# Optimization experiments

Hardware: AMD Instinct MI355X
Metric: run time of the kernel (lower is better)

The kernel has to match this reference:

```python
import jax, jax.numpy as jnp
import numpy as np

N = 50000        # nodes
E = 1600000      # edges (avg degree 32)
D = 64           # emb_dim
H = 2            # heads
NEG_SLOPE = 0.2
BOND_VOCAB = 5   # vocab per bond feature (3 categorical features)


def setup_inputs() -> dict:
    key = jax.random.key(0)
    ks = jax.random.split(key, 8)
    x = jax.random.normal(ks[0], (N, D), jnp.float32)
    edge_index = jax.random.randint(ks[1], (2, E), 0, N)
    edge_attr = jax.random.randint(ks[2], (E, 3), 0, BOND_VOCAB)
    W = jax.random.normal(ks[3], (D, H * D), jnp.float32) / np.float32(np.sqrt(D))
    b_W = jnp.zeros((H * D,), jnp.float32)
    att = jax.random.normal(ks[4], (1, H, 2 * D), jnp.float32) * 0.1
    bias = jnp.zeros((D,), jnp.float32)
    bond_emb = jax.random.normal(ks[5], (3, BOND_VOCAB, H * D), jnp.float32) * 0.1
    return dict(x=x, edge_index=edge_index, edge_attr=edge_attr,
                W=W, b_W=b_W, att=att, bias=bias, bond_emb=bond_emb)


def reference(x, edge_index, edge_attr, W, b_W, att, bias, bond_emb):
    row, col = edge_index[0], edge_index[1]  # src (x_j), dst (x_i / aggregation target)
    # BondEncoder: sum of per-feature categorical embeddings -> [E, H*D]
    e = (bond_emb[0][edge_attr[:, 0]]
         + bond_emb[1][edge_attr[:, 1]]
         + bond_emb[2][edge_attr[:, 2]])
    h = x @ W + b_W                                   # [N, H*D]
    x_j = h[row].reshape(-1, H, D) + e.reshape(-1, H, D)   # message source + edge emb
    x_i = h[col].reshape(-1, H, D)                         # message target
    # attention logits: [E, H]
    alpha = (jnp.concatenate([x_i, x_j], axis=-1) * att).sum(-1)
    alpha = jnp.where(alpha >= 0, alpha, NEG_SLOPE * alpha)  # leaky_relu
    # segment softmax over edge_index[0] (source node), PyG semantics
    m = jax.ops.segment_max(alpha, row, num_segments=N)      # [N, H]
    m = jnp.where(jnp.isfinite(m), m, 0.0)                   # empty segments -> 0
    ea = jnp.exp(alpha - m[row])
    s = jax.ops.segment_sum(ea, row, num_segments=N)
    alpha = ea / (s[row] + 1e-16)
    # weighted messages, scatter-add to destination nodes
    msg = x_j * alpha[:, :, None]                            # [E, H, D]
    aggr = jax.ops.segment_sum(msg, col, num_segments=N)     # [N, H, D]
    # update: mean over heads + bias
    return aggr.mean(axis=1) + bias
```

## Files before the change

### kernel.cpp

```cpp
#include <hip/hip_runtime.h>
#include <hip/hip_bf16.h>
#include <math.h>

#define NEG_SLOPE 0.2f
#define CHUNK 2048
#define NPB2 128
#define SCAP 5120

__device__ __forceinline__ unsigned f2bf(float f) {
  unsigned u = __float_as_uint(f);
  return (u + 0x7fffu + ((u >> 16) & 1u)) >> 16;
}

__global__ __launch_bounds__(256) void k1_gemm(
    const float* __restrict__ x, const float* __restrict__ W,
    const float* __restrict__ bW, const float* __restrict__ att,
    unsigned int* __restrict__ hb, float* __restrict__ ai,
    float* __restrict__ aj, int Nn) {
  int t = threadIdx.x;
  int lane = t & 63;
  int wid = blockIdx.x * (blockDim.x >> 6) + (t >> 6);
  int nwaves = gridDim.x * (blockDim.x >> 6);

  float Wr0[64], Wr1[64];
#pragma unroll
  for (int k = 0; k < 64; ++k) {
    Wr0[k] = W[k * 128 + lane];
    Wr1[k] = W[k * 128 + 64 + lane];
  }
  float bs0 = bW[lane], bs1 = bW[64 + lane];
  float ati0 = att[lane];
  float atj0 = att[64 + lane];
  float ati1 = att[128 + lane];
  float atj1 = att[192 + lane];

  for (int row = wid; row < Nn; row += nwaves) {
    int r = __builtin_amdgcn_readfirstlane(row);
    const float* __restrict__ xr = x + (size_t)r * 64;
    float a0a = 0.f, a0b = 0.f, a1a = 0.f, a1b = 0.f;
#pragma unroll
    for (int k = 0; k < 64; k += 2) {
      float xk0 = xr[k], xk1 = xr[k + 1];
      a0a = fmaf(xk0, Wr0[k], a0a);
      a1a = fmaf(xk0, Wr1[k], a1a);
      a0b = fmaf(xk1, Wr0[k + 1], a0b);
      a1b = fmaf(xk1, Wr1[k + 1], a1b);
    }
    float h0 = a0a + a0b + bs0;
    float h1 = a1a + a1b + bs1;
    hb[(size_t)r * 64 + lane] = f2bf(h0) | (f2bf(h1) << 16);

    float ti0 = ati0 * h0, tj0 = atj0 * h0;
    float ti1 = ati1 * h1, tj1 = atj1 * h1;
    ti0 += __shfl_xor(ti0, 32, 64);
    tj0 += __shfl_xor(tj0, 32, 64);
    ti1 += __shfl_xor(ti1, 32, 64);
    tj1 += __shfl_xor(tj1, 32, 64);
    float mi = (lane < 32) ? ti0 : ti1;
    float mj = (lane < 32) ? tj0 : tj1;
#pragma unroll
    for (int off = 16; off > 0; off >>= 1) {
      mi += __shfl_xor(mi, off, 64);
      mj += __shfl_xor(mj, off, 64);
    }
    if ((lane & 31) == 0) {
      ai[r * 2 + (lane >> 5)] = mi;
      aj[r * 2 + (lane >> 5)] = mj;
    }
  }
}

__global__ __launch_bounds__(256) void k_bin(
    const int* __restrict__ ei, const int* __restrict__ eattr,
    unsigned int* __restrict__ rec, int* __restrict__ cnt_tbl,
    int* __restrict__ base_tbl, unsigned int* __restrict__ rec_src,
    int* __restrict__ cnt_tbl2, int* __restrict__ base_tbl2, int Ee, int NCB) {
  __shared__ unsigned sbuf[CHUNK];
  __shared__ unsigned sbuf2[CHUNK];
  __shared__ int hist[512], cur[512], hist2[512], cur2[512];
  int t = threadIdx.x;
  for (int i = t; i < NCB; i += 256) { hist[i] = 0; hist2[i] = 0; }
  __syncthreads();
  int start = blockIdx.x * CHUNK;
  int end = min(start + CHUNK, Ee);
  int cnt = end - start;
  int cbv[CHUNK / 256], cb2v[CHUNK / 256];
  unsigned pkv[CHUNK / 256], pk2v[CHUNK / 256];
  int nk = 0;
  for (int e = start + t; e < end; e += 256, ++nk) {
    int dst = __builtin_nontemporal_load(&ei[Ee + e]);
    int src = __builtin_nontemporal_load(&ei[e]);
    int a0 = __builtin_nontemporal_load(&eattr[e * 3]);
    int a1 = __builtin_nontemporal_load(&eattr[e * 3 + 1]);
    int a2 = __builtin_nontemporal_load(&eattr[e * 3 + 2]);
    unsigned c012 = (unsigned)(a0 + 5 * a1 + 25 * a2);
    cbv[nk] = dst >> 7;
    pkv[nk] = (unsigned)src | (c012 << 16) | ((unsigned)(dst & 127) << 23);
    cb2v[nk] = src >> 7;
    pk2v[nk] = (unsigned)dst | ((unsigned)(src & 127) << 17) | (c012 << 24);
    atomicAdd(&hist[dst >> 7], 1);
    atomicAdd(&hist2[src >> 7], 1);
  }
  __syncthreads();
  if (t == 0) {
    int s = 0;
    for (int i = 0; i < NCB; ++i) { cur[i] = s; s += hist[i]; }
  }
  if (t == 64) {
    int s = 0;
    for (int i = 0; i < NCB; ++i) { cur2[i] = s; s += hist2[i]; }
  }
  __syncthreads();
  for (int i = t; i < NCB; i += 256) {
    cnt_tbl[blockIdx.x * NCB + i] = hist[i];
    base_tbl[blockIdx.x * NCB + i] = cur[i];
    cnt_tbl2[blockIdx.x * NCB + i] = hist2[i];
    base_tbl2[blockIdx.x * NCB + i] = cur2[i];
  }
  __syncthreads();
  for (int k = 0; k < nk; ++k) {
    int pos = atomicAdd(&cur[cbv[k]], 1);
    sbuf[pos] = pkv[k];
    int pos2 = atomicAdd(&cur2[cb2v[k]], 1);
    sbuf2[pos2] = pk2v[k];
  }
  __syncthreads();
  for (int i = t; i < cnt; i += 256) {
    __builtin_nontemporal_store(sbuf[i], &rec[start + i]);
    __builtin_nontemporal_store(sbuf2[i], &rec_src[start + i]);
  }
}

__global__ __launch_bounds__(256) void k_segoff_a(
    const int* __restrict__ cnt_tbl, int* __restrict__ segdst,
    int* __restrict__ btot, int NCB, int NBLK) {
  __shared__ int s[256];
  int t = threadIdx.x, cb = blockIdx.x;
  int per = (NBLK + 255) / 256;
  int loc[8];
  int sum = 0;
  for (int j = 0; j < per; ++j) {
    int blk = t * per + j;
    int v = (blk < NBLK) ? cnt_tbl[blk * NCB + cb] : 0;
    loc[j] = sum;
    sum += v;
  }
  s[t] = sum;
  __syncthreads();
#pragma unroll
  for (int o = 1; o < 256; o <<= 1) {
    int xv = (t >= o) ? s[t - o] : 0;
    __syncthreads();
    s[t] += xv;
    __syncthreads();
  }
  int excl = s[t] - sum;
  for (int j = 0; j < per; ++j) {
    int blk = t * per + j;
    if (blk < NBLK) segdst[cb * NBLK + blk] = excl + loc[j];
  }
  if (t == 255) btot[cb] = s[255];
}

__global__ __launch_bounds__(512) void k_segoff_b(
    const int* __restrict__ btot, int* __restrict__ coarse_base, int NCB, int Ee) {
  __shared__ int s[512];
  int t = threadIdx.x;
  int v = (t < NCB) ? btot[t] : 0;
  s[t] = v;
  __syncthreads();
#pragma unroll
  for (int o = 1; o < 512; o <<= 1) {
    int xv = (t >= o) ? s[t - o] : 0;
    __syncthreads();
    s[t] += xv;
    __syncthreads();
  }
  if (t < NCB) coarse_base[t] = s[t] - v;
  if (t == 0) coarse_base[NCB] = Ee;
}

__global__ __launch_bounds__(256) void k_sacc(
    const unsigned int* __restrict__ rec_src, const int* __restrict__ cnt_tbl2,
    const int* __restrict__ base_tbl2, const int* __restrict__ segdst2,
    const int* __restrict__ btot2, const float2* __restrict__ ai2,
    const float2* __restrict__ aj2, const float* __restrict__ att,
    const float* __restrict__ bemb, float* __restrict__ sden,
    int Nn, int NCB, int NBLK) {
  __shared__ unsigned ubuf[SCAP];
  __shared__ float sdl[NPB2 * 2];
  __shared__ float2 ajs[NPB2];
  __shared__ float tbl[30];
  int t = threadIdx.x;
  int cb = blockIdx.x;
  if (t < 30) {
    int f = t / 10, rem = t % 10, c = rem >> 1, hh = rem & 1;
    float sacc = 0.f;
    for (int d = 0; d < 64; ++d)
      sacc += att[hh * 128 + 64 + d] * bemb[(f * 5 + c) * 128 + hh * 64 + d];
    tbl[t] = sacc;
  }
  int node0 = cb << 7;
  if (t < NPB2 && node0 + t < Nn) ajs[t] = aj2[node0 + t];
  sdl[t] = 0.f;
  int total = btot2[cb];
  __syncthreads();
  bool fits = (total <= SCAP);

#define SACC_BODY(U, AIV)                                                      \
  {                                                                            \
    int sl = ((U) >> 17) & 127;                                                \
    int c012 = ((U) >> 24) & 127;                                              \
    int a0 = c012 % 5, a1 = (c012 / 5) % 5, a2 = c012 / 25;                    \
    float2 ajv = ajs[sl];                                                      \
    float lg0 = AIV.x + ajv.x + tbl[a0 * 2] + tbl[10 + a1 * 2] +               \
                tbl[20 + a2 * 2];                                              \
    float lg1 = AIV.y + ajv.y + tbl[a0 * 2 + 1] + tbl[10 + a1 * 2 + 1] +       \
                tbl[20 + a2 * 2 + 1];                                          \
    lg0 = lg0 >= 0.f ? lg0 : NEG_SLOPE * lg0;                                  \
    lg1 = lg1 >= 0.f ? lg1 : NEG_SLOPE * lg1;                                  \
    atomicAdd(&sdl[sl * 2], __expf(lg0));                                      \
    atomicAdd(&sdl[sl * 2 + 1], __expf(lg1));                                  \
  }

  if (fits) {
    for (int blk = t; blk < NBLK; blk += 256) {
      int len = cnt_tbl2[blk * NCB + cb];
      if (!len) continue;
      int sp = blk * CHUNK + base_tbl2[blk * NCB + cb];
      int dp = segdst2[cb * NBLK + blk];
      for (int j = 0; j < len; ++j) ubuf[dp + j] = rec_src[sp + j];
    }
    __syncthreads();
    int i = t;
    for (; i + 3 * 256 < total; i += 4 * 256) {
      unsigned u[4];
      float2 aiv[4];
#pragma unroll
      for (int k = 0; k < 4; ++k) u[k] = ubuf[i + k * 256];
#pragma unroll
      for (int k = 0; k < 4; ++k) aiv[k] = ai2[u[k] & 0x1FFFF];
#pragma unroll
      for (int k = 0; k < 4; ++k) SACC_BODY(u[k], aiv[k])
    }
    for (; i < total; i += 256) {
      unsigned u = ubuf[i];
      float2 aiv = ai2[u & 0x1FFFF];
      SACC_BODY(u, aiv)
    }
  } else {
    for (int blk = t; blk < NBLK; blk += 256) {
      int len = cnt_tbl2[blk * NCB + cb];
      int sp = blk * CHUNK + base_tbl2[blk * NCB + cb];
      for (int j = 0; j < len; ++j) {
        unsigned u = rec_src[sp + j];
        float2 aiv = ai2[u & 0x1FFFF];
        SACC_BODY(u, aiv)
      }
    }
  }
#undef SACC_BODY
  __syncthreads();
  if (node0 + (t >> 1) < Nn) sden[(size_t)node0 * 2 + t] = sdl[t];
}

__global__ __launch_bounds__(256) void k_sort(
    const unsigned int* __restrict__ rec, const int* __restrict__ cnt_tbl,
    const int* __restrict__ base_tbl, const int* __restrict__ segdst,
    const int* __restrict__ coarse_base, const float2* __restrict__ ai2,
    const float2* __restrict__ aj2, const float2* __restrict__ sd2,
    const float* __restrict__ att, const float* __restrict__ bemb,
    unsigned int* __restrict__ eix2, float2* __restrict__ alpha2,
    int* __restrict__ off, int Nn, int NCB, int NBLK, int Ee) {
  __shared__ unsigned ubuf[SCAP];
  __shared__ unsigned ubuf2[SCAP];
  __shared__ int hist[NPB2], basex[NPB2], curx[NPB2];
  __shared__ float tbl[30];
  __shared__ float2 ais[NPB2];
  int t = threadIdx.x;
  int cb = blockIdx.x;
  if (t < 30) {
    int f = t / 10, rem = t % 10, c = rem >> 1, hh = rem & 1;
    float sacc = 0.f;
    for (int d = 0; d < 64; ++d)
      sacc += att[hh * 128 + 64 + d] * bemb[(f * 5 + c) * 128 + hh * 64 + d];
    tbl[t] = sacc;
  }
  int node0 = cb << 7;
  if (t < NPB2) {
    hist[t] = 0;
    if (node0 + t < Nn) ais[t] = ai2[node0 + t];
  }
  int gbase = coarse_base[cb];
  int total = coarse_base[cb + 1] - gbase;
  __syncthreads();
  bool fits = (total <= SCAP);

  if (fits) {
    for (int blk = t; blk < NBLK; blk += 256) {
      int len = cnt_tbl[blk * NCB + cb];
      if (!len) continue;
      int sp = blk * CHUNK + base_tbl[blk * NCB + cb];
      int dp = segdst[cb * NBLK + blk];
      for (int j = 0; j < len; ++j) ubuf[dp + j] = rec[sp + j];
    }
    __syncthreads();
    for (int i = t; i < total; i += 256)
      atomicAdd(&hist[(ubuf[i] >> 23) & 127], 1);
    __syncthreads();
    if (t == 0) {
      int s = 0;
      for (int i = 0; i < NPB2; ++i) { basex[i] = s; s += hist[i]; }
    }
    __syncthreads();
    if (t < NPB2) {
      curx[t] = basex[t];
      if (node0 + t < Nn) off[node0 + t] = gbase + basex[t];
    }
    if (cb == 0 && t == 0) off[Nn] = Ee;
    __syncthreads();
    for (int i = t; i < total; i += 256) {
      unsigned u = ubuf[i];
      int pos = atomicAdd(&curx[(u >> 23) & 127], 1);
      ubuf2[pos] = u;
    }
    __syncthreads();

#define OUT_BODY(I, U, AJV, SDV)                                               \
    {                                                                          \
      int src = (U) & 0xFFFF;                                                  \
      int c012 = ((U) >> 16) & 127;                                            \
      int dl = ((U) >> 23) & 127;                                              \
      int a0 = c012 % 5, a1 = (c012 / 5) % 5, a2 = c012 / 25;                  \
      float2 aiv = ais[dl];                                                    \
      float lg0 = aiv.x + AJV.x + tbl[a0 * 2] + tbl[10 + a1 * 2] +             \
                  tbl[20 + a2 * 2];                                            \
      float lg1 = aiv.y + AJV.y + tbl[a0 * 2 + 1] + tbl[10 + a1 * 2 + 1] +     \
                  tbl[20 + a2 * 2 + 1];                                        \
      lg0 = lg0 >= 0.f ? lg0 : NEG_SLOPE * lg0;                                \
      lg1 = lg1 >= 0.f ? lg1 : NEG_SLOPE * lg1;                                \
      eix2[gbase + (I)] = (unsigned)src | ((unsigned)a0 << 16) |               \
                          ((unsigned)a1 << 19) | ((unsigned)a2 << 22);         \
      alpha2[gbase + (I)] = make_float2(__expf(lg0) / (SDV.x + 1e-16f),        \
                                        __expf(lg1) / (SDV.y + 1e-16f));       \
    }

    int i = t;
    for (; i + 3 * 256 < total; i += 4 * 256) {
      unsigned u[4];
      float2 ajv[4], sdv[4];
#pragma unroll
      for (int k = 0; k < 4; ++k) u[k] = ubuf2[i + k * 256];
#pragma unroll
      for (int k = 0; k < 4; ++k) ajv[k] = aj2[u[k] & 0xFFFF];
#pragma unroll
      for (int k = 0; k < 4; ++k) sdv[k] = sd2[u[k] & 0xFFFF];
#pragma unroll
      for (int k = 0; k < 4; ++k) OUT_BODY(i + k * 256, u[k], ajv[k], sdv[k])
    }
    for (; i < total; i += 256) {
      unsigned u = ubuf2[i];
      float2 ajv = aj2[u & 0xFFFF];
      float2 sdv = sd2[u & 0xFFFF];
      OUT_BODY(i, u, ajv, sdv)
    }
#undef OUT_BODY
  } else {
    for (int blk = t; blk < NBLK; blk += 256) {
      int len = cnt_tbl[blk * NCB + cb];
      int sp = blk * CHUNK + base_tbl[blk * NCB + cb];
      for (int j = 0; j < len; ++j)
        atomicAdd(&hist[(rec[sp + j] >> 23) & 127], 1);
    }
    __syncthreads();
    if (t == 0) {
      int s = 0;
      for (int i = 0; i < NPB2; ++i) { basex[i] = s; s += hist[i]; }
    }
    __syncthreads();
    if (t < NPB2) {
      curx[t] = basex[t];
      if (node0 + t < Nn) off[node0 + t] = gbase + basex[t];
    }
    if (cb == 0 && t == 0) off[Nn] = Ee;
    __syncthreads();
    for (int blk = t; blk < NBLK; blk += 256) {
      int len = cnt_tbl[blk * NCB + cb];
      int sp = blk * CHUNK + base_tbl[blk * NCB + cb];
      for (int j = 0; j < len; ++j) {
        unsigned u = rec[sp + j];
        int src = u & 0xFFFF;
        int c012 = (u >> 16) & 127;
        int dl = (u >> 23) & 127;
        int a0 = c012 % 5, a1 = (c012 / 5) % 5, a2 = c012 / 25;
        float2 aiv = ais[dl];
        float2 ajv = aj2[src];
        float2 sdv = sd2[src];
        float lg0 = aiv.x + ajv.x + tbl[a0 * 2] + tbl[10 + a1 * 2] + tbl[20 + a2 * 2];
        float lg1 = aiv.y + ajv.y + tbl[a0 * 2 + 1] + tbl[10 + a1 * 2 + 1] +
                    tbl[20 + a2 * 2 + 1];
        lg0 = lg0 >= 0.f ? lg0 : NEG_SLOPE * lg0;
        lg1 = lg1 >= 0.f ? lg1 : NEG_SLOPE * lg1;
        int pos = gbase + atomicAdd(&curx[dl], 1);
        eix2[pos] = (unsigned)src | ((unsigned)a0 << 16) | ((unsigned)a1 << 19) |
                    ((unsigned)a2 << 22);
        alpha2[pos] = make_float2(__expf(lg0) / (sdv.x + 1e-16f),
                                  __expf(lg1) / (sdv.y + 1e-16f));
      }
    }
  }
}

__global__ __launch_bounds__(256) void k_gather(
    const unsigned int* __restrict__ eix, const float2* __restrict__ alpha2,
    const int* __restrict__ off, const unsigned int* __restrict__ hb,
    const float* __restrict__ bemb, const float* __restrict__ bias,
    float* __restrict__ out, int Nn) {
  __shared__ float bembs[15 * 128];
  __shared__ float wsm[4][32];
  int t = threadIdx.x;
  for (int i = t; i < 15 * 128; i += 256) bembs[i] = bemb[i];
  __syncthreads();
  int wave = t >> 6, lane = t & 63;
  int n = blockIdx.x * 4 + wave;
  if (n >= Nn) return;
  int p0 = __builtin_amdgcn_readfirstlane(off[n]);
  int p1 = __builtin_amdgcn_readfirstlane(off[n + 1]);
  int myf = lane / 5;
  int myc = lane % 5;
  bool active = lane < 15;
  float w0 = 0.f, w1 = 0.f;
  float acc0 = 0.f, acc1 = 0.f;

#define EDGE_BODY(U, HV, AL)                                                   \
  {                                                                            \
    acc0 = fmaf(AL.x, __uint_as_float((HV) << 16), acc0);                      \
    acc1 = fmaf(AL.y, __uint_as_float((HV) & 0xffff0000u), acc1);              \
    int a0 = ((U) >> 16) & 7, a1 = ((U) >> 19) & 7, a2 = ((U) >> 22) & 7;      \
    int sel = myf == 0 ? a0 : (myf == 1 ? a1 : a2);                            \
    float m = (active && myc == sel) ? 1.0f : 0.0f;                            \
    w0 = fmaf(m, AL.x, w0);                                                    \
    w1 = fmaf(m, AL.y, w1);                                                    \
  }

  int p = p0;
  for (; p + 8 <= p1; p += 8) {
    unsigned u[8], hv[8];
    float2 al[8];
#pragma unroll
    for (int k = 0; k < 8; ++k) u[k] = eix[p + k];
#pragma unroll
    for (int k = 0; k < 8; ++k) al[k] = alpha2[p + k];
#pragma unroll
    for (int k = 0; k < 8; ++k) {
      const unsigned* __restrict__ hrow = hb + ((size_t)(u[k] & 0xFFFFu) << 6);
      hv[k] = hrow[lane];
    }
#pragma unroll
    for (int k = 0; k < 8; ++k) EDGE_BODY(u[k], hv[k], al[k])
  }
  for (; p < p1; ++p) {
    unsigned u0 = eix[p];
    float2 al0 = alpha2[p];
    const unsigned* __restrict__ hrow = hb + ((size_t)(u0 & 0xFFFFu) << 6);
    unsigned hv0 = hrow[lane];
    EDGE_BODY(u0, hv0, al0)
  }
#undef EDGE_BODY

  if (active) {
    wsm[wave][lane * 2] = w0;
    wsm[wave][lane * 2 + 1] = w1;
  }
#pragma unroll
  for (int k = 0; k < 15; ++k) {
    acc0 += wsm[wave][k * 2] * bembs[k * 128 + lane];
    acc1 += wsm[wave][k * 2 + 1] * bembs[k * 128 + 64 + lane];
  }
  out[(size_t)n * 64 + lane] = 0.5f * (acc0 + acc1) + bias[lane];
}

extern "C" void kernel_launch(void* const* d_in, const int* in_sizes, int n_in,
                              void* d_out, int out_size, void* d_ws, size_t ws_size,
                              hipStream_t stream) {
  const float* x    = (const float*)d_in[0];
  const int*   ei   = (const int*)d_in[1];
  const int*   eatt = (const int*)d_in[2];
  const float* W    = (const float*)d_in[3];
  const float* bW   = (const float*)d_in[4];
  const float* att  = (const float*)d_in[5];
  const float* bias = (const float*)d_in[6];
  const float* bemb = (const float*)d_in[7];
  int Nn = in_sizes[0] / 64;
  int Ee = in_sizes[1] / 2;
  int NCB = (Nn + NPB2 - 1) / NPB2;
  int NBLK = (Ee + CHUNK - 1) / CHUNK;

  char* ws = (char*)d_ws;
  ws = (char*)(((uintptr_t)ws + 15) & ~(uintptr_t)15);
  float* aj = (float*)ws;                 ws += (size_t)Nn * 2 * 4;
  float* sden = (float*)ws;               ws += (size_t)Nn * 2 * 4;
  float* ai = (float*)ws;                 ws += (size_t)Nn * 2 * 4;
  unsigned int* hb = (unsigned int*)ws;   ws += (size_t)Nn * 64 * 4;
  unsigned int* rec = (unsigned int*)ws;  ws += (size_t)NBLK * CHUNK * 4;
  unsigned int* rec_src = (unsigned int*)ws; ws += (size_t)NBLK * CHUNK * 4;
  unsigned int* eix2 = (unsigned int*)ws; ws += (size_t)Ee * 4;
  float2* alpha2 = (float2*)ws;           ws += (size_t)Ee * 8;
  int* off = (int*)ws;                    ws += (size_t)(Nn + 1) * 4;
  int* cnt_tbl = (int*)ws;                ws += (size_t)NBLK * NCB * 4;
  int* base_tbl = (int*)ws;               ws += (size_t)NBLK * NCB * 4;
  int* cnt_tbl2 = (int*)ws;               ws += (size_t)NBLK * NCB * 4;
  int* base_tbl2 = (int*)ws;              ws += (size_t)NBLK * NCB * 4;
  int* segdst = (int*)ws;                 ws += (size_t)NCB * NBLK * 4;
  int* segdst2 = (int*)ws;                ws += (size_t)NCB * NBLK * 4;
  int* coarse_base = (int*)ws;            ws += (size_t)(NCB + 1) * 4;
  int* btot = (int*)ws;                   ws += (size_t)NCB * 4;
  int* btot2 = (int*)ws;                  ws += (size_t)NCB * 4;

  k1_gemm<<<1024, 256, 0, stream>>>(x, W, bW, att, hb, ai, aj, Nn);
  k_bin<<<NBLK, 256, 0, stream>>>(ei, eatt, rec, cnt_tbl, base_tbl, rec_src,
                                  cnt_tbl2, base_tbl2, Ee, NCB);
  k_segoff_a<<<NCB, 256, 0, stream>>>(cnt_tbl, segdst, btot, NCB, NBLK);
  k_segoff_a<<<NCB, 256, 0, stream>>>(cnt_tbl2, segdst2, btot2, NCB, NBLK);
  k_segoff_b<<<1, 512, 0, stream>>>(btot, coarse_base, NCB, Ee);
  k_sacc<<<NCB, 256, 0, stream>>>(rec_src, cnt_tbl2, base_tbl2, segdst2, btot2,
                                  (const float2*)ai, (const float2*)aj, att,
                                  bemb, sden, Nn, NCB, NBLK);
  k_sort<<<NCB, 256, 0, stream>>>(rec, cnt_tbl, base_tbl, segdst, coarse_base,
                                  (const float2*)ai, (const float2*)aj,
                                  (const float2*)sden, att, bemb, eix2, alpha2,
                                  off, Nn, NCB, NBLK, Ee);
  k_gather<<<(Nn + 3) / 4, 256, 0, stream>>>(eix2, alpha2, off, hb, bemb, bias,
                                             (float*)d_out, Nn);
}
```

Baseline: 284.8 us.

## Fuse softmax denominator into binning kernel via global atomics, drop source-sorted pass

Removes the second (source-keyed) binning, its segment-offset pass and the separate k_sacc kernel. Instead, k_bin computes each edge's attention logits and atomically adds the exponentials into a zero-initialised global denominator array. The aim is to cut a kernel launch plus the extra record writes and reads. The cost is 3.2M global float atomics with random addresses. It also doubles CHUNK to 4096, halving the number of bin blocks and table sizes, and simplifies the bond-mask selection in the gather loop.

After: 398.8 us. +40.0%, slower.

```diff
diff --git a/kernel.cpp b/kernel.cpp
--- a/kernel.cpp
+++ b/kernel.cpp
@@ -3,7 +3,7 @@
 #include <math.h>
 
 #define NEG_SLOPE 0.2f
-#define CHUNK 2048
+#define CHUNK 4096
 #define NPB2 128
 #define SCAP 5120
 
@@ -72,20 +72,28 @@
 
 __global__ __launch_bounds__(256) void k_bin(
     const int* __restrict__ ei, const int* __restrict__ eattr,
+    const float2* __restrict__ ai2, const float2* __restrict__ aj2,
+    const float* __restrict__ att, const float* __restrict__ bemb,
     unsigned int* __restrict__ rec, int* __restrict__ cnt_tbl,
-    int* __restrict__ base_tbl, unsigned int* __restrict__ rec_src,
-    int* __restrict__ cnt_tbl2, int* __restrict__ base_tbl2, int Ee, int NCB) {
+    int* __restrict__ base_tbl, float* __restrict__ sden, int Ee, int NCB) {
   __shared__ unsigned sbuf[CHUNK];
-  __shared__ unsigned sbuf2[CHUNK];
-  __shared__ int hist[512], cur[512], hist2[512], cur2[512];
+  __shared__ int hist[512], cur[512];
+  __shared__ float tbl[30];
   int t = threadIdx.x;
-  for (int i = t; i < NCB; i += 256) { hist[i] = 0; hist2[i] = 0; }
+  if (t < 30) {
+    int f = t / 10, rem = t % 10, c = rem >> 1, hh = rem & 1;
+    float sacc = 0.f;
+    for (int d = 0; d < 64; ++d)
+      sacc += att[hh * 128 + 64 + d] * bemb[(f * 5 + c) * 128 + hh * 64 + d];
+    tbl[t] = sacc;
+  }
+  for (int i = t; i < NCB; i += 256) hist[i] = 0;
   __syncthreads();
   int start = blockIdx.x * CHUNK;
   int end = min(start + CHUNK, Ee);
   int cnt = end - start;
-  int cbv[CHUNK / 256], cb2v[CHUNK / 256];
-  unsigned pkv[CHUNK / 256], pk2v[CHUNK / 256];
+  int cbv[CHUNK / 256];
+  unsigned pkv[CHUNK / 256];
   int nk = 0;
   for (int e = start + t; e < end; e += 256, ++nk) {
     int dst = __builtin_nontemporal_load(&ei[Ee + e]);
@@ -96,39 +104,35 @@
     unsigned c012 = (unsigned)(a0 + 5 * a1 + 25 * a2);
     cbv[nk] = dst >> 7;
     pkv[nk] = (unsigned)src | (c012 << 16) | ((unsigned)(dst & 127) << 23);
-    cb2v[nk] = src >> 7;
-    pk2v[nk] = (unsigned)dst | ((unsigned)(src & 127) << 17) | (c012 << 24);
     atomicAdd(&hist[dst >> 7], 1);
-    atomicAdd(&hist2[src >> 7], 1);
+    float2 aiv = ai2[dst];
+    float2 ajv = aj2[src];
+    float lg0 = aiv.x + ajv.x + tbl[a0 * 2] + tbl[10 + a1 * 2] + tbl[20 + a2 * 2];
+    float lg1 = aiv.y + ajv.y + tbl[a0 * 2 + 1] + tbl[10 + a1 * 2 + 1] +
+                tbl[20 + a2 * 2 + 1];
+    lg0 = lg0 >= 0.f ? lg0 : NEG_SLOPE * lg0;
+    lg1 = lg1 >= 0.f ? lg1 : NEG_SLOPE * lg1;
+    atomicAdd(&sden[src * 2], __expf(lg0));
+    atomicAdd(&sden[src * 2 + 1], __expf(lg1));
   }
   __syncthreads();
   if (t == 0) {
     int s = 0;
     for (int i = 0; i < NCB; ++i) { cur[i] = s; s += hist[i]; }
   }
-  if (t == 64) {
-    int s = 0;
-    for (int i = 0; i < NCB; ++i) { cur2[i] = s; s += hist2[i]; }
-  }
   __syncthreads();
   for (int i = t; i < NCB; i += 256) {
     cnt_tbl[blockIdx.x * NCB + i] = hist[i];
     base_tbl[blockIdx.x * NCB + i] = cur[i];
-    cnt_tbl2[blockIdx.x * NCB + i] = hist2[i];
-    base_tbl2[blockIdx.x * NCB + i] = cur2[i];
   }
   __syncthreads();
   for (int k = 0; k < nk; ++k) {
     int pos = atomicAdd(&cur[cbv[k]], 1);
     sbuf[pos] = pkv[k];
-    int pos2 = atomicAdd(&cur2[cb2v[k]], 1);
-    sbuf2[pos2] = pk2v[k];
-  }
-  __syncthreads();
-  for (int i = t; i < cnt; i += 256) {
+  }
+  __syncthreads();
+  for (int i = t; i < cnt; i += 256)
     __builtin_nontemporal_store(sbuf[i], &rec[start + i]);
-    __builtin_nontemporal_store(sbuf2[i], &rec_src[start + i]);
-  }
 }
 
 __global__ __launch_bounds__(256) void k_segoff_a(
@@ -178,90 +182,6 @@
   }
   if (t < NCB) coarse_base[t] = s[t] - v;
   if (t == 0) coarse_base[NCB] = Ee;
-}
-
-__global__ __launch_bounds__(256) void k_sacc(
-    const unsigned int* __restrict__ rec_src, const int* __restrict__ cnt_tbl2,
-    const int* __restrict__ base_tbl2, const int* __restrict__ segdst2,
-    const int* __restrict__ btot2, const float2* __restrict__ ai2,
-    const float2* __restrict__ aj2, const float* __restrict__ att,
-    const float* __restrict__ bemb, float* __restrict__ sden,
-    int Nn, int NCB, int NBLK) {
-  __shared__ unsigned ubuf[SCAP];
-  __shared__ float sdl[NPB2 * 2];
-  __shared__ float2 ajs[NPB2];
-  __shared__ float tbl[30];
-  int t = threadIdx.x;
-  int cb = blockIdx.x;
-  if (t < 30) {
-    int f = t / 10, rem = t % 10, c = rem >> 1, hh = rem & 1;
-    float sacc = 0.f;
-    for (int d = 0; d < 64; ++d)
-      sacc += att[hh * 128 + 64 + d] * bemb[(f * 5 + c) * 128 + hh * 64 + d];
-    tbl[t] = sacc;
-  }
-  int node0 = cb << 7;
-  if (t < NPB2 && node0 + t < Nn) ajs[t] = aj2[node0 + t];
-  sdl[t] = 0.f;
-  int total = btot2[cb];
-  __syncthreads();
-  bool fits = (total <= SCAP);
-
-#define SACC_BODY(U, AIV)                                                      \
-  {                                                                            \
-    int sl = ((U) >> 17) & 127;                                                \
-    int c012 = ((U) >> 24) & 127;                                              \
-    int a0 = c012 % 5, a1 = (c012 / 5) % 5, a2 = c012 / 25;                    \
-    float2 ajv = ajs[sl];                                                      \
-    float lg0 = AIV.x + ajv.x + tbl[a0 * 2] + tbl[10 + a1 * 2] +               \
-                tbl[20 + a2 * 2];                                              \
-    float lg1 = AIV.y + ajv.y + tbl[a0 * 2 + 1] + tbl[10 + a1 * 2 + 1] +       \
-                tbl[20 + a2 * 2 + 1];                                          \
-    lg0 = lg0 >= 0.f ? lg0 : NEG_SLOPE * lg0;                                  \
-    lg1 = lg1 >= 0.f ? lg1 : NEG_SLOPE * lg1;                                  \
-    atomicAdd(&sdl[sl * 2], __expf(lg0));                                      \
-    atomicAdd(&sdl[sl * 2 + 1], __expf(lg1));                                  \
-  }
-
-  if (fits) {
-    for (int blk = t; blk < NBLK; blk += 256) {
-      int len = cnt_tbl2[blk * NCB + cb];
-      if (!len) continue;
-      int sp = blk * CHUNK + base_tbl2[blk * NCB + cb];
-      int dp = segdst2[cb * NBLK + blk];
-      for (int j = 0; j < len; ++j) ubuf[dp + j] = rec_src[sp + j];
-    }
-    __syncthreads();
-    int i = t;
-    for (; i + 3 * 256 < total; i += 4 * 256) {
-      unsigned u[4];
-      float2 aiv[4];
-#pragma unroll
-      for (int k = 0; k < 4; ++k) u[k] = ubuf[i + k * 256];
-#pragma unroll
-      for (int k = 0; k < 4; ++k) aiv[k] = ai2[u[k] & 0x1FFFF];
-#pragma unroll
-      for (int k = 0; k < 4; ++k) SACC_BODY(u[k], aiv[k])
-    }
-    for (; i < total; i += 256) {
-      unsigned u = ubuf[i];
-      float2 aiv = ai2[u & 0x1FFFF];
-      SACC_BODY(u, aiv)
-    }
-  } else {
-    for (int blk = t; blk < NBLK; blk += 256) {
-      int len = cnt_tbl2[blk * NCB + cb];
-      int sp = blk * CHUNK + base_tbl2[blk * NCB + cb];
-      for (int j = 0; j < len; ++j) {
-        unsigned u = rec_src[sp + j];
-        float2 aiv = ai2[u & 0x1FFFF];
-        SACC_BODY(u, aiv)
-      }
-    }
-  }
-#undef SACC_BODY
-  __syncthreads();
-  if (node0 + (t >> 1) < Nn) sden[(size_t)node0 * 2 + t] = sdl[t];
 }
 
 __global__ __launch_bounds__(256) void k_sort(
@@ -429,6 +349,8 @@
   int myf = lane / 5;
   int myc = lane % 5;
   bool active = lane < 15;
+  int myshift = 16 + 3 * myf;
+  int mycEff = active ? myc : 8;
   float w0 = 0.f, w1 = 0.f;
   float acc0 = 0.f, acc1 = 0.f;
 
@@ -436,9 +358,8 @@
   {                                                                            \
     acc0 = fmaf(AL.x, __uint_as_float((HV) << 16), acc0);                      \
     acc1 = fmaf(AL.y, __uint_as_float((HV) & 0xffff0000u), acc1);              \
-    int a0 = ((U) >> 16) & 7, a1 = ((U) >> 19) & 7, a2 = ((U) >> 22) & 7;      \
-    int sel = myf == 0 ? a0 : (myf == 1 ? a1 : a2);                            \
-    float m = (active && myc == sel) ? 1.0f : 0.0f;                            \
+    int sel = (int)(((U) >> myshift) & 7u);                                    \
+    float m = (sel == mycEff) ? 1.0f : 0.0f;                                   \
     w0 = fmaf(m, AL.x, w0);                                                    \
     w1 = fmaf(m, AL.y, w1);                                                    \
   }
@@ -503,29 +424,22 @@
   float* ai = (float*)ws;                 ws += (size_t)Nn * 2 * 4;
   unsigned int* hb = (unsigned int*)ws;   ws += (size_t)Nn * 64 * 4;
   unsigned int* rec = (unsigned int*)ws;  ws += (size_t)NBLK * CHUNK * 4;
-  unsigned int* rec_src = (unsigned int*)ws; ws += (size_t)NBLK * CHUNK * 4;
   unsigned int* eix2 = (unsigned int*)ws; ws += (size_t)Ee * 4;
   float2* alpha2 = (float2*)ws;           ws += (size_t)Ee * 8;
   int* off = (int*)ws;                    ws += (size_t)(Nn + 1) * 4;
   int* cnt_tbl = (int*)ws;                ws += (size_t)NBLK * NCB * 4;
   int* base_tbl = (int*)ws;               ws += (size_t)NBLK * NCB * 4;
-  int* cnt_tbl2 = (int*)ws;               ws += (size_t)NBLK * NCB * 4;
-  int* base_tbl2 = (int*)ws;              ws += (size_t)NBLK * NCB * 4;
   int* segdst = (int*)ws;                 ws += (size_t)NCB * NBLK * 4;
-  int* segdst2 = (int*)ws;                ws += (size_t)NCB * NBLK * 4;
   int* coarse_base = (int*)ws;            ws += (size_t)(NCB + 1) * 4;
   int* btot = (int*)ws;                   ws += (size_t)NCB * 4;
-  int* btot2 = (int*)ws;                  ws += (size_t)NCB * 4;
-
+
+  hipMemsetAsync(sden, 0, (size_t)Nn * 2 * 4, stream);
   k1_gemm<<<1024, 256, 0, stream>>>(x, W, bW, att, hb, ai, aj, Nn);
-  k_bin<<<NBLK, 256, 0, stream>>>(ei, eatt, rec, cnt_tbl, base_tbl, rec_src,
-                                  cnt_tbl2, base_tbl2, Ee, NCB);
+  k_bin<<<NBLK, 256, 0, stream>>>(ei, eatt, (const float2*)ai,
+                                  (const float2*)aj, att, bemb, rec, cnt_tbl,
+                                  base_tbl, sden, Ee, NCB);
   k_segoff_a<<<NCB, 256, 0, stream>>>(cnt_tbl, segdst, btot, NCB, NBLK);
-  k_segoff_a<<<NCB, 256, 0, stream>>>(cnt_tbl2, segdst2, btot2, NCB, NBLK);
   k_segoff_b<<<1, 512, 0, stream>>>(btot, coarse_base, NCB, Ee);
-  k_sacc<<<NCB, 256, 0, stream>>>(rec_src, cnt_tbl2, base_tbl2, segdst2, btot2,
-                                  (const float2*)ai, (const float2*)aj, att,
-                                  bemb, sden, Nn, NCB, NBLK);
   k_sort<<<NCB, 256, 0, stream>>>(rec, cnt_tbl, base_tbl, segdst, coarse_base,
                                   (const float2*)ai, (const float2*)aj,
                                   (const float2*)sden, att, bemb, eix2, alpha2,
```
